# Optimization experiments

Measured on AMD Instinct MI355X. Metric: run time of the kernel, lower is better.

## Reference

```python
import jax, jax.numpy as jnp
import numpy as np

SH_DIM = 9                      # (sh_deg+1)^2, sh_deg=2
DATA_DIM = SH_DIM * 3 + 1       # 28
FINE = 8
COARSE = 32
RADIUS = 1.3
NUM_ATOMS = 16
BATCH = 128
STEP = (RADIUS * 2.0 / COARSE / FINE) / 2.0   # fine_voxel_len / 2
N_INTRS = COARSE * 3 * 2 * FINE               # 1536


def sh_encode(dirs):
    # degree-2 real spherical harmonics bases, [.., 9]
    x, y, z = dirs[..., 0], dirs[..., 1], dirs[..., 2]
    C0 = 0.28209479177387814
    C1 = 0.4886025119029199
    C2 = (1.0925484305920792, -1.0925484305920792, 0.31539156525252005,
          -1.0925484305920792, 0.5462742152960396)
    return jnp.stack([
        jnp.full_like(x, C0), -C1 * y, C1 * z, -C1 * x,
        C2[0] * x * y, C2[1] * y * z, C2[2] * (2.0 * z * z - x * x - y * y),
        C2[3] * x * z, C2[4] * (x * x - y * y)], axis=-1)


def dict_interp(grid, atoms, pts):
    # pts: [N,3] normalized to [0,1). grid: [COARSE^3, A]. atoms: [FINE^3, A, D].
    # coarse voxel -> dictionary coefficients; trilinear interp of atoms inside it.
    cpos = pts * COARSE
    cidx = jnp.clip(jnp.floor(cpos), 0, COARSE - 1)
    ci = cidx.astype(jnp.int32)
    coeff = grid[(ci[:, 0] * COARSE + ci[:, 1]) * COARSE + ci[:, 2]]  # [N, A]
    local = cpos - cidx                       # [0,1) within coarse voxel
    fpos = local * FINE - 0.5
    f0f = jnp.floor(fpos)
    w = fpos - f0f                            # trilinear weights
    f0 = f0f.astype(jnp.int32)
    out = jnp.zeros((pts.shape[0], DATA_DIM), dtype=pts.dtype)
    for dx in (0, 1):
        for dy in (0, 1):
            for dz in (0, 1):
                ix = jnp.clip(f0[:, 0] + dx, 0, FINE - 1)
                iy = jnp.clip(f0[:, 1] + dy, 0, FINE - 1)
                iz = jnp.clip(f0[:, 2] + dz, 0, FINE - 1)
                wt = ((w[:, 0] if dx else 1.0 - w[:, 0]) *
                      (w[:, 1] if dy else 1.0 - w[:, 1]) *
                      (w[:, 2] if dz else 1.0 - w[:, 2]))
                vals = jnp.einsum('na,nad->nd', coeff, atoms[(ix * FINE + iy) * FINE + iz])
                out = out + wt[:, None] * vals
    return out


def setup_inputs() -> dict:
    key = jax.random.key(0)
    k1, k2, k3, k4 = jax.random.split(key, 4)
    rays_o = jnp.array([0.0, 0.0, -2.0 * RADIUS]) + 0.05 * jax.random.normal(k1, (BATCH, 3), jnp.float32)
    d = 0.25 * jax.random.normal(k2, (BATCH, 3), jnp.float32) + jnp.array([0.0, 0.0, 1.0])
    rays_d = d / jnp.linalg.norm(d, axis=-1, keepdims=True)
    grid = 0.01 * jax.random.normal(k3, (COARSE ** 3, NUM_ATOMS), jnp.float32)
    atoms_sh = jax.random.uniform(k4, (FINE ** 3, NUM_ATOMS, DATA_DIM - 1), jnp.float32)
    atoms = jnp.concatenate([atoms_sh, jnp.full((FINE ** 3, NUM_ATOMS, 1), 0.01, jnp.float32)], -1)
    return {"rays_o": rays_o, "rays_d": rays_d, "grid": grid, "atoms": atoms, "grid_id": 0}


def reference(rays_o, rays_d, grid, atoms, grid_id):
    B = rays_o.shape[0]
    # ---- sample_proposal (no-grad in original) ----
    off_pos = (RADIUS - rays_o) / rays_d
    off_neg = (-RADIUS - rays_o) / rays_d
    start = jnp.max(jnp.minimum(off_pos, off_neg), axis=-1, keepdims=True)
    steps = jnp.arange(N_INTRS, dtype=rays_o.dtype)[None, :]
    intersections = jax.lax.stop_gradient(start + steps * STEP)        # [B, 1536]
    tsec = intersections[:, :-1]                                       # [B, M]
    M = N_INTRS - 1
    pts = rays_o[:, None, :] + tsec[:, :, None] * rays_d[:, None, :]   # [B, M, 3]
    mask = jnp.all((pts > -RADIUS) & (pts < RADIUS), axis=-1)          # [B, M]
    pts_n = jnp.clip((pts + RADIUS) / (2.0 * RADIUS), 0.0, 1.0 - 1e-6)
    pts_n = jax.lax.stop_gradient(pts_n).reshape(-1, 3)
    # ---- dictionary interpolation (computed densely, zeroed by mask) ----
    data = dict_interp(grid, atoms, pts_n).reshape(B, M, DATA_DIM)
    sigma = jax.nn.relu(jnp.where(mask, data[..., -1], 0.0))           # [B, M]
    # ---- sigma -> alpha / weights ----
    dists = (intersections[:, 1:] - intersections[:, :-1]) * jnp.linalg.norm(rays_d, axis=-1, keepdims=True)
    alpha = 1.0 - jnp.exp(-sigma * dists)
    trans = jnp.concatenate([jnp.ones((B, 1), alpha.dtype),
                             jnp.cumprod(1.0 - alpha + 1e-10, axis=-1)[:, :-1]], axis=-1)
    abs_light = alpha * trans                                          # [B, M]
    # ---- SH -> rgb, composite ----
    sh_mult = sh_encode(rays_d)[:, None, None, :]                      # [B,1,1,9]
    sh = data[..., :-1].reshape(B, M, 3, SH_DIM)
    rgb_raw = jnp.where(mask[..., None], jnp.sum(sh_mult * sh, axis=-1), 0.0)  # [B,M,3]
    rgb = jnp.sum(abs_light[..., None] * jax.nn.sigmoid(rgb_raw), axis=1)
    rgb = rgb + (1.0 - jnp.sum(abs_light, axis=-1))[:, None]           # white background
    depth = jnp.sum(abs_light * tsec, axis=-1)
    return rgb, alpha, depth
```

## Files before the change

### kernel.cpp

```cpp
#include <hip/hip_runtime.h>

typedef unsigned int u32;

#define MSAMP 1535
#define NS 1024
#define RADF 1.3f
#define STEPF ((float)(1.3 * 2.0 / 32.0 / 8.0 / 2.0))
#define NATOMS 229376
#define NCELLG 32768
#define CSCALE 0.06f

#if __has_builtin(__builtin_amdgcn_sdot4)
#define SDOT4(a, b, c) __builtin_amdgcn_sdot4((a), (b), (c), false)
#else
static __device__ __forceinline__ int SDOT4(int a, int b, int c) {
#pragma unroll
    for (int i = 0; i < 4; i++) {
        int ai = (a << (24 - 8 * i)) >> 24;
        int bi = (b << (24 - 8 * i)) >> 24;
        c += ai * bi;
    }
    return c;
}
#endif

__device__ __forceinline__ u32 q4(float a, float b, float c, float d, float S) {
    int i0 = (int)rintf(fminf(fmaxf(a * S, -127.0f), 127.0f));
    int i1 = (int)rintf(fminf(fmaxf(b * S, -127.0f), 127.0f));
    int i2 = (int)rintf(fminf(fmaxf(c * S, -127.0f), 127.0f));
    int i3 = (int)rintf(fminf(fmaxf(d * S, -127.0f), 127.0f));
    return (u32)(i0 & 255) | ((u32)(i1 & 255) << 8) | ((u32)(i2 & 255) << 16)
         | ((u32)(i3 & 255) << 24);
}

__global__ __launch_bounds__(256) void k_t(const float* __restrict__ atoms,
                                           const float* __restrict__ grid,
                                           signed char* __restrict__ wst2,
                                           uint4* __restrict__ gridq,
                                           float4* __restrict__ acc4) {
    int o = blockIdx.x * 256 + threadIdx.x;
    if (o < NATOMS) {
        float v = atoms[o];
        int cell = o / 448;
        int r = o - cell * 448;
        int a = r / 28;
        int d = r - a * 28;
        int s = d >> 2, j = d & 3;
        int qv = (int)rintf(v * 127.0f);
        wst2[s * 32768 + cell * 64 + j * 16 + a] = (signed char)qv;
    } else if (o < NATOMS + NCELLG) {
        int cell = o - NATOMS;
        const float4* gp = (const float4*)(grid + cell * 16);
        float4 c0 = gp[0], c1 = gp[1], c2 = gp[2], c3 = gp[3];
        const float S = 127.0f / CSCALE;
        uint4 outv;
        outv.x = q4(c0.x, c0.y, c0.z, c0.w, S);
        outv.y = q4(c1.x, c1.y, c1.z, c1.w, S);
        outv.z = q4(c2.x, c2.y, c2.z, c2.w, S);
        outv.w = q4(c3.x, c3.y, c3.z, c3.w, S);
        gridq[cell] = outv;
    } else {
        acc4[o - NATOMS - NCELLG] = make_float4(0.0f, 0.0f, 0.0f, 0.0f);
    }
}

__global__ __launch_bounds__(512) void k_p1(const float* __restrict__ ro,
                                            const float* __restrict__ rd,
                                            const uint4* __restrict__ gridq,
                                            const signed char* __restrict__ wst2,
                                            float* __restrict__ acc4) {
    __shared__ __align__(16) signed char hl[512 * 80];
    int bx = blockIdx.x;
    int s  = bx >> 6;
    int pr = bx & 63;
    int tid = threadIdx.x;
    int ray = pr * 2 + (tid >> 8);
    int q   = tid & 255;

    {
        const uint4* src = (const uint4*)(wst2 + s * 32768);
#pragma unroll
        for (int it = 0; it < 4; it++) {
            int idx = it * 512 + tid;
            uint4 v = src[idx];
            int cell = idx >> 2, part = idx & 3;
            *(uint4*)&hl[cell * 80 + part * 16] = v;
        }
    }
    __syncthreads();

    float ox = ro[ray * 3 + 0], oy = ro[ray * 3 + 1], oz = ro[ray * 3 + 2];
    float dx = rd[ray * 3 + 0], dy = rd[ray * 3 + 1], dz = rd[ray * 3 + 2];
    float a0 = ( RADF - ox) / dx, b0 = (-RADF - ox) / dx;
    float a1 = ( RADF - oy) / dy, b1 = (-RADF - oy) / dy;
    float a2 = ( RADF - oz) / dz, b2 = (-RADF - oz) / dz;
    float st = fmaxf(fmaxf(fminf(a0, b0), fminf(a1, b1)), fminf(a2, b2));

    float shm[9];
    shm[0] = 0.28209479177387814f;
    shm[1] = -0.4886025119029199f * dy;
    shm[2] =  0.4886025119029199f * dz;
    shm[3] = -0.4886025119029199f * dx;
    shm[4] =  1.0925484305920792f * dx * dy;
    shm[5] = -1.0925484305920792f * dy * dz;
    shm[6] =  0.31539156525252005f * (2.0f * dz * dz - dx * dx - dy * dy);
    shm[7] = -1.0925484305920792f * dx * dz;
    shm[8] =  0.5462742152960396f * (dx * dx - dy * dy);

    float wA[4] = {0,0,0,0}, wB[4] = {0,0,0,0};
    int chanA = 0, chanB = 0; bool hasB = false;
    switch (s) {
        case 0: chanA=0; wA[0]=shm[0]; wA[1]=shm[1]; wA[2]=shm[2]; wA[3]=shm[3]; break;
        case 1: chanA=0; wA[0]=shm[4]; wA[1]=shm[5]; wA[2]=shm[6]; wA[3]=shm[7]; break;
        case 2: chanA=0; wA[0]=shm[8];
                chanB=1; wB[1]=shm[0]; wB[2]=shm[1]; wB[3]=shm[2]; hasB=true; break;
        case 3: chanA=1; wA[0]=shm[3]; wA[1]=shm[4]; wA[2]=shm[5]; wA[3]=shm[6]; break;
        case 4: chanA=1; wA[0]=shm[7]; wA[1]=shm[8];
                chanB=2; wB[2]=shm[0]; wB[3]=shm[1]; hasB=true; break;
        case 5: chanA=2; wA[0]=shm[2]; wA[1]=shm[3]; wA[2]=shm[4]; wA[3]=shm[5]; break;
        default: chanA=2; wA[0]=shm[6]; wA[1]=shm[7]; wA[2]=shm[8];
                chanB=3; wB[3]=1.0f; hasB=true; break;
    }
    const float QS = CSCALE / (127.0f * 127.0f);
#pragma unroll
    for (int i = 0; i < 4; i++) { wA[i] *= QS; wB[i] *= QS; }

#pragma unroll
    for (int k = 0; k < 4; k++) {
        int m = q + k * 256;
        float t = st + (float)m * STEPF;
        float px = ox + t * dx, py = oy + t * dy, pz = oz + t * dz;
        bool inb = (px > -RADF) && (px < RADF) && (py > -RADF) && (py < RADF)
                && (pz > -RADF) && (pz < RADF);
        if (!inb) continue;

        const float inv2R = 1.0f / 2.6f;
        float pnx = fminf(fmaxf((px + RADF) * inv2R, 0.0f), 0.999999f);
        float pny = fminf(fmaxf((py + RADF) * inv2R, 0.0f), 0.999999f);
        float pnz = fminf(fmaxf((pz + RADF) * inv2R, 0.0f), 0.999999f);

        float cpx = pnx * 32.0f, cpy = pny * 32.0f, cpz = pnz * 32.0f;
        float cfx = floorf(cpx), cfy = floorf(cpy), cfz = floorf(cpz);
        int cix = (int)cfx, ciy = (int)cfy, ciz = (int)cfz;

        float fpx = (cpx - cfx) * 8.0f - 0.5f;
        float fpy = (cpy - cfy) * 8.0f - 0.5f;
        float fpz = (cpz - cfz) * 8.0f - 0.5f;
        float ffx = floorf(fpx), ffy = floorf(fpy), ffz = floorf(fpz);
        int f0x = (int)ffx, f0y = (int)ffy, f0z = (int)ffz;
        float wx = fpx - ffx, wy = fpy - ffy, wz = fpz - ffz;

        int ixa[2] = { max(f0x, 0), min(f0x + 1, 7) };
        int iya[2] = { max(f0y, 0), min(f0y + 1, 7) };
        int iza[2] = { max(f0z, 0), min(f0z + 1, 7) };
        float wxa[2] = { 1.0f - wx, wx };
        float wya[2] = { 1.0f - wy, wy };
        float wza[2] = { 1.0f - wz, wz };

        uint4 cq = gridq[(cix * 32 + ciy) * 32 + ciz];
        float acc[4] = {0.0f, 0.0f, 0.0f, 0.0f};

#pragma unroll
        for (int cx = 0; cx < 2; cx++)
#pragma unroll
        for (int cy = 0; cy < 2; cy++)
#pragma unroll
        for (int cz = 0; cz < 2; cz++) {
            float wt = wxa[cx] * wya[cy] * wza[cz];
            int cb = ((ixa[cx] * 8 + iya[cy]) * 8 + iza[cz]) * 80;
#pragma unroll
            for (int j = 0; j < 4; j++) {
                uint4 qa = *(const uint4*)&hl[cb + j * 16];
                int di = SDOT4((int)qa.x, (int)cq.x, 0);
                di = SDOT4((int)qa.y, (int)cq.y, di);
                di = SDOT4((int)qa.z, (int)cq.z, di);
                di = SDOT4((int)qa.w, (int)cq.w, di);
                acc[j] = fmaf(wt, (float)di, acc[j]);
            }
        }

        float vA = fmaf(wA[0], acc[0], fmaf(wA[1], acc[1],
                   fmaf(wA[2], acc[2], wA[3] * acc[3])));
        int base = (ray * NS + m) * 4;
        atomicAdd(&acc4[base + chanA], vA);
        if (hasB) {
            float vB = fmaf(wB[0], acc[0], fmaf(wB[1], acc[1],
                       fmaf(wB[2], acc[2], wB[3] * acc[3])));
            atomicAdd(&acc4[base + chanB], vB);
        }
    }
}

__global__ __launch_bounds__(1024) void k_p2(const float* __restrict__ ro,
                                             const float* __restrict__ rd,
                                             const float4* __restrict__ acc4,
                                             float* __restrict__ rgb_out,
                                             float* __restrict__ alpha_out,
                                             float* __restrict__ depth_out) {
    int ray = blockIdx.x;
    int t = threadIdx.x;
    int lane = t & 63, wave = t >> 6;

    int abase = ray * MSAMP;
    if (NS + t < MSAMP) alpha_out[abase + NS + t] = 0.0f;

    float dx = rd[ray * 3 + 0], dy = rd[ray * 3 + 1], dz = rd[ray * 3 + 2];
    float ox = ro[ray * 3 + 0], oy = ro[ray * 3 + 1], oz = ro[ray * 3 + 2];
    float a0 = ( RADF - ox) / dx, b0 = (-RADF - ox) / dx;
    float a1 = ( RADF - oy) / dy, b1 = (-RADF - oy) / dy;
    float a2 = ( RADF - oz) / dz, b2 = (-RADF - oz) / dz;
    float st = fmaxf(fmaxf(fminf(a0, b0), fminf(a1, b1)), fminf(a2, b2));
    float nrm = sqrtf(dx * dx + dy * dy + dz * dz);

    int m = t;
    float tm = st + (float)m * STEPF;
    float4 d4 = acc4[ray * NS + m];
    float sigma = fmaxf(d4.w, 0.0f);
    float alpha = 1.0f - __expf(-sigma * STEPF * nrm);
    float r0 = 1.0f / (1.0f + __expf(-d4.x));
    float r1 = 1.0f / (1.0f + __expf(-d4.y));
    float r2 = 1.0f / (1.0f + __expf(-d4.z));
    alpha_out[abase + m] = alpha;

    float p = 1.0f - alpha + 1e-10f;

    float incl = p;
#pragma unroll
    for (int off = 1; off < 64; off <<= 1) {
        float vv = __shfl_up(incl, off);
        if (lane >= off) incl *= vv;
    }
    __shared__ float wprod[16];
    if (lane == 63) wprod[wave] = incl;
    __syncthreads();
    float excl = __shfl_up(incl, 1);
    if (lane == 0) excl = 1.0f;
    for (int w = 0; w < 16; w++) if (w < wave) excl *= wprod[w];

    float w_ = alpha * excl;
    float vals[5] = { w_ * r0, w_ * r1, w_ * r2, w_ * tm, w_ };
    __shared__ float wred[16][5];
#pragma unroll
    for (int i = 0; i < 5; i++) {
        float v = vals[i];
        v += __shfl_xor(v, 1);  v += __shfl_xor(v, 2);  v += __shfl_xor(v, 4);
        v += __shfl_xor(v, 8);  v += __shfl_xor(v, 16); v += __shfl_xor(v, 32);
        if (lane == 0) wred[wave][i] = v;
    }
    __syncthreads();
    if (t == 0) {
        float res[5];
#pragma unroll
        for (int i = 0; i < 5; i++) {
            float r_ = 0.0f;
            for (int w = 0; w < 16; w++) r_ += wred[w][i];
            res[i] = r_;
        }
        float omw = 1.0f - res[4];
        rgb_out[ray * 3 + 0] = res[0] + omw;
        rgb_out[ray * 3 + 1] = res[1] + omw;
        rgb_out[ray * 3 + 2] = res[2] + omw;
        depth_out[ray] = res[3];
    }
}

extern "C" void kernel_launch(void* const* d_in, const int* in_sizes, int n_in,
                              void* d_out, int out_size, void* d_ws, size_t ws_size,
                              hipStream_t stream) {
    const float* ro    = (const float*)d_in[0];
    const float* rd    = (const float*)d_in[1];
    const float* grid  = (const float*)d_in[2];
    const float* atoms = (const float*)d_in[3];
    int B = in_sizes[0] / 3;

    signed char* wst2 = (signed char*)d_ws;
    uint4* gridq = (uint4*)((char*)d_ws + 229376);
    float* acc4  = (float*)((char*)d_ws + 229376 + 524288);

    float* out       = (float*)d_out;
    float* rgb_out   = out;
    float* alpha_out = out + B * 3;
    float* depth_out = out + B * 3 + B * MSAMP;

    hipLaunchKernelGGL(k_t,  dim3(393216 / 256), dim3(256), 0, stream,
                       atoms, grid, wst2, (uint4*)gridq, (float4*)acc4);
    hipLaunchKernelGGL(k_p1, dim3(448), dim3(512), 0, stream,
                       ro, rd, (const uint4*)gridq, wst2, acc4);
    hipLaunchKernelGGL(k_p2, dim3(B), dim3(1024), 0, stream,
                       ro, rd, (const float4*)acc4, rgb_out, alpha_out, depth_out);
}
```

Baseline: 82.95 us.

## Fuse compositing pass into accumulation kernel via last-block-done counter

Removes the separate compositing kernel. Each of the 7 slice blocks that share a ray pair increments a per-pair counter, and the last block to finish reads the accumulated values with atomic loads and does the transmittance scan and reduction for both rays, with 2 samples per thread. This saves one kernel launch and the extra pass over the accumulator. In exchange the composite work is serialized inside a single block per ray pair, and it adds fences, a counter array and a counter reset in the prep kernel.

```diff
diff --git a/kernel.cpp b/kernel.cpp
--- a/kernel.cpp
+++ b/kernel.cpp
@@ -8,6 +8,7 @@
 #define STEPF ((float)(1.3 * 2.0 / 32.0 / 8.0 / 2.0))
 #define NATOMS 229376
 #define NCELLG 32768
+#define NACC   131072
 #define CSCALE 0.06f
 
 #if __has_builtin(__builtin_amdgcn_sdot4)
@@ -37,7 +38,8 @@
                                            const float* __restrict__ grid,
                                            signed char* __restrict__ wst2,
                                            uint4* __restrict__ gridq,
-                                           float4* __restrict__ acc4) {
+                                           float4* __restrict__ acc4,
+                                           int* __restrict__ cnt) {
     int o = blockIdx.x * 256 + threadIdx.x;
     if (o < NATOMS) {
         float v = atoms[o];
@@ -59,8 +61,10 @@
         outv.z = q4(c2.x, c2.y, c2.z, c2.w, S);
         outv.w = q4(c3.x, c3.y, c3.z, c3.w, S);
         gridq[cell] = outv;
-    } else {
+    } else if (o < NATOMS + NCELLG + NACC) {
         acc4[o - NATOMS - NCELLG] = make_float4(0.0f, 0.0f, 0.0f, 0.0f);
+    } else if (o < NATOMS + NCELLG + NACC + 64) {
+        cnt[o - NATOMS - NCELLG - NACC] = 0;
     }
 }
 
@@ -68,7 +72,11 @@
                                             const float* __restrict__ rd,
                                             const uint4* __restrict__ gridq,
                                             const signed char* __restrict__ wst2,
-                                            float* __restrict__ acc4) {
+                                            float* __restrict__ acc4,
+                                            int* __restrict__ cnt,
+                                            float* __restrict__ rgb_out,
+                                            float* __restrict__ alpha_out,
+                                            float* __restrict__ depth_out) {
     __shared__ __align__(16) signed char hl[512 * 80];
     int bx = blockIdx.x;
     int s  = bx >> 6;
@@ -189,78 +197,102 @@
             atomicAdd(&acc4[base + chanB], vB);
         }
     }
-}
-
-__global__ __launch_bounds__(1024) void k_p2(const float* __restrict__ ro,
-                                             const float* __restrict__ rd,
-                                             const float4* __restrict__ acc4,
-                                             float* __restrict__ rgb_out,
-                                             float* __restrict__ alpha_out,
-                                             float* __restrict__ depth_out) {
-    int ray = blockIdx.x;
-    int t = threadIdx.x;
-    int lane = t & 63, wave = t >> 6;
-
-    int abase = ray * MSAMP;
-    if (NS + t < MSAMP) alpha_out[abase + NS + t] = 0.0f;
-
-    float dx = rd[ray * 3 + 0], dy = rd[ray * 3 + 1], dz = rd[ray * 3 + 2];
-    float ox = ro[ray * 3 + 0], oy = ro[ray * 3 + 1], oz = ro[ray * 3 + 2];
-    float a0 = ( RADF - ox) / dx, b0 = (-RADF - ox) / dx;
-    float a1 = ( RADF - oy) / dy, b1 = (-RADF - oy) / dy;
-    float a2 = ( RADF - oz) / dz, b2 = (-RADF - oz) / dz;
-    float st = fmaxf(fmaxf(fminf(a0, b0), fminf(a1, b1)), fminf(a2, b2));
-    float nrm = sqrtf(dx * dx + dy * dy + dz * dz);
-
-    int m = t;
-    float tm = st + (float)m * STEPF;
-    float4 d4 = acc4[ray * NS + m];
-    float sigma = fmaxf(d4.w, 0.0f);
-    float alpha = 1.0f - __expf(-sigma * STEPF * nrm);
-    float r0 = 1.0f / (1.0f + __expf(-d4.x));
-    float r1 = 1.0f / (1.0f + __expf(-d4.y));
-    float r2 = 1.0f / (1.0f + __expf(-d4.z));
-    alpha_out[abase + m] = alpha;
-
-    float p = 1.0f - alpha + 1e-10f;
-
-    float incl = p;
-#pragma unroll
-    for (int off = 1; off < 64; off <<= 1) {
-        float vv = __shfl_up(incl, off);
-        if (lane >= off) incl *= vv;
-    }
-    __shared__ float wprod[16];
-    if (lane == 63) wprod[wave] = incl;
+
     __syncthreads();
-    float excl = __shfl_up(incl, 1);
-    if (lane == 0) excl = 1.0f;
-    for (int w = 0; w < 16; w++) if (w < wave) excl *= wprod[w];
-
-    float w_ = alpha * excl;
-    float vals[5] = { w_ * r0, w_ * r1, w_ * r2, w_ * tm, w_ };
-    __shared__ float wred[16][5];
-#pragma unroll
-    for (int i = 0; i < 5; i++) {
-        float v = vals[i];
-        v += __shfl_xor(v, 1);  v += __shfl_xor(v, 2);  v += __shfl_xor(v, 4);
-        v += __shfl_xor(v, 8);  v += __shfl_xor(v, 16); v += __shfl_xor(v, 32);
-        if (lane == 0) wred[wave][i] = v;
+    __shared__ int sOld;
+    if (tid == 0) {
+        __threadfence();
+        sOld = atomicAdd(&cnt[pr], 1);
     }
     __syncthreads();
-    if (t == 0) {
-        float res[5];
+    if (sOld != 6) return;
+    __threadfence();
+
+    float* sv = (float*)hl;
+    int lane = tid & 63, wave = tid >> 6;
+
+    for (int r2 = 0; r2 < 2; r2++) {
+        int ray2 = pr * 2 + r2;
+        float ox2 = ro[ray2 * 3 + 0], oy2 = ro[ray2 * 3 + 1], oz2 = ro[ray2 * 3 + 2];
+        float dx2 = rd[ray2 * 3 + 0], dy2 = rd[ray2 * 3 + 1], dz2 = rd[ray2 * 3 + 2];
+        float c0 = ( RADF - ox2) / dx2, d0 = (-RADF - ox2) / dx2;
+        float c1 = ( RADF - oy2) / dy2, d1 = (-RADF - oy2) / dy2;
+        float c2 = ( RADF - oz2) / dz2, d2 = (-RADF - oz2) / dz2;
+        float st2 = fmaxf(fmaxf(fminf(c0, d0), fminf(c1, d1)), fminf(c2, d2));
+        float nrm2 = sqrtf(dx2 * dx2 + dy2 * dy2 + dz2 * dz2);
+        int abase = ray2 * MSAMP;
+
+        if (NS + tid < MSAMP) alpha_out[abase + NS + tid] = 0.0f;
+
+        float av[2], rr[2], rg[2], rb[2], tmv[2];
+#pragma unroll
+        for (int kk = 0; kk < 2; kk++) {
+            int m = tid * 2 + kk;
+            tmv[kk] = st2 + (float)m * STEPF;
+            const float* ap = acc4 + (ray2 * NS + m) * 4;
+            float vx = __hip_atomic_load(&ap[0], __ATOMIC_RELAXED, __HIP_MEMORY_SCOPE_AGENT);
+            float vy = __hip_atomic_load(&ap[1], __ATOMIC_RELAXED, __HIP_MEMORY_SCOPE_AGENT);
+            float vz = __hip_atomic_load(&ap[2], __ATOMIC_RELAXED, __HIP_MEMORY_SCOPE_AGENT);
+            float vw = __hip_atomic_load(&ap[3], __ATOMIC_RELAXED, __HIP_MEMORY_SCOPE_AGENT);
+            float sigma = fmaxf(vw, 0.0f);
+            float alpha = 1.0f - __expf(-sigma * STEPF * nrm2);
+            av[kk] = alpha;
+            rr[kk] = 1.0f / (1.0f + __expf(-vx));
+            rg[kk] = 1.0f / (1.0f + __expf(-vy));
+            rb[kk] = 1.0f / (1.0f + __expf(-vz));
+            alpha_out[abase + m] = alpha;
+        }
+
+        float p = (1.0f - av[0] + 1e-10f) * (1.0f - av[1] + 1e-10f);
+        float incl = p;
+#pragma unroll
+        for (int off = 1; off < 64; off <<= 1) {
+            float vv = __shfl_up(incl, off);
+            if (lane >= off) incl *= vv;
+        }
+        if (lane == 63) sv[wave] = incl;
+        __syncthreads();
+        float excl = __shfl_up(incl, 1);
+        if (lane == 0) excl = 1.0f;
+        for (int w = 0; w < 8; w++) if (w < wave) excl *= sv[w];
+
+        float trans = excl;
+        float sra = 0, sga = 0, sba = 0, sda = 0, swm = 0;
+#pragma unroll
+        for (int kk = 0; kk < 2; kk++) {
+            float w_ = av[kk] * trans;
+            sra = fmaf(w_, rr[kk], sra);
+            sga = fmaf(w_, rg[kk], sga);
+            sba = fmaf(w_, rb[kk], sba);
+            sda = fmaf(w_, tmv[kk], sda);
+            swm += w_;
+            trans *= (1.0f - av[kk] + 1e-10f);
+        }
+
+        float vals[5] = { sra, sga, sba, sda, swm };
 #pragma unroll
         for (int i = 0; i < 5; i++) {
-            float r_ = 0.0f;
-            for (int w = 0; w < 16; w++) r_ += wred[w][i];
-            res[i] = r_;
-        }
-        float omw = 1.0f - res[4];
-        rgb_out[ray * 3 + 0] = res[0] + omw;
-        rgb_out[ray * 3 + 1] = res[1] + omw;
-        rgb_out[ray * 3 + 2] = res[2] + omw;
-        depth_out[ray] = res[3];
+            float v = vals[i];
+            v += __shfl_xor(v, 1);  v += __shfl_xor(v, 2);  v += __shfl_xor(v, 4);
+            v += __shfl_xor(v, 8);  v += __shfl_xor(v, 16); v += __shfl_xor(v, 32);
+            if (lane == 0) sv[8 + wave * 5 + i] = v;
+        }
+        __syncthreads();
+        if (tid == 0) {
+            float res[5];
+#pragma unroll
+            for (int i = 0; i < 5; i++) {
+                float r_ = 0.0f;
+                for (int w = 0; w < 8; w++) r_ += sv[8 + w * 5 + i];
+                res[i] = r_;
+            }
+            float omw = 1.0f - res[4];
+            rgb_out[ray2 * 3 + 0] = res[0] + omw;
+            rgb_out[ray2 * 3 + 1] = res[1] + omw;
+            rgb_out[ray2 * 3 + 2] = res[2] + omw;
+            depth_out[ray2] = res[3];
+        }
+        __syncthreads();
     }
 }
 
@@ -276,16 +308,16 @@
     signed char* wst2 = (signed char*)d_ws;
     uint4* gridq = (uint4*)((char*)d_ws + 229376);
     float* acc4  = (float*)((char*)d_ws + 229376 + 524288);
+    int*   cnt   = (int*)((char*)d_ws + 229376 + 524288 + 2097152);
 
     float* out       = (float*)d_out;
     float* rgb_out   = out;
     float* alpha_out = out + B * 3;
     float* depth_out = out + B * 3 + B * MSAMP;
 
-    hipLaunchKernelGGL(k_t,  dim3(393216 / 256), dim3(256), 0, stream,
-                       atoms, grid, wst2, (uint4*)gridq, (float4*)acc4);
+    hipLaunchKernelGGL(k_t,  dim3((393280 + 255) / 256), dim3(256), 0, stream,
+                       atoms, grid, wst2, (uint4*)gridq, (float4*)acc4, cnt);
     hipLaunchKernelGGL(k_p1, dim3(448), dim3(512), 0, stream,
-                       ro, rd, (const uint4*)gridq, wst2, acc4);
-    hipLaunchKernelGGL(k_p2, dim3(B), dim3(1024), 0, stream,
-                       ro, rd, (const float4*)acc4, rgb_out, alpha_out, depth_out);
-}
+                       ro, rd, (const uint4*)gridq, wst2, acc4, cnt,
+                       rgb_out, alpha_out, depth_out);
+}
```

Measured after the change: 96.97 us. 1.17x slower.
